# Kernel tuning notes

Measured on AMD Instinct MI355X. Metric: run time of the kernel, lower is better.

The kernel has to match this reference:

```python
import jax, jax.numpy as jnp
import numpy as np

N_NODES = 50000
N_EDGES = 600000
IN_C = 128
OUT_C = 128
N_REL = 8


def setup_inputs() -> dict:
    key = jax.random.key(0)
    k1, k2, k3, k4 = jax.random.split(key, 4)
    x = jax.random.normal(k1, (N_NODES, IN_C), dtype=jnp.float32)
    edge_index = jax.random.randint(k2, (2, N_EDGES), 0, N_NODES, dtype=jnp.int64)
    edge_type = jax.random.randint(k3, (N_EDGES,), 0, N_REL, dtype=jnp.int64)
    weight = jax.random.normal(k4, (N_REL, IN_C, OUT_C), dtype=jnp.float32)
    bias = jnp.zeros((OUT_C,), dtype=jnp.float32)
    return {"x": x, "edge_index": edge_index, "edge_type": edge_type,
            "weight": weight, "bias": bias}


def reference(x, edge_index, edge_type, weight, bias):
    # x: [N, in], edge_index: [2, E] (src, dst), edge_type: [E]
    # weight: [R, in, out], bias: [out]
    N = x.shape[0]
    src = edge_index[0]
    dst = edge_index[1]
    out = jnp.zeros((N, weight.shape[2]), dtype=x.dtype)
    for r in range(weight.shape[0]):
        rel_mask = (edge_type == r).astype(x.dtype)  # [E]
        transformed = x @ weight[r]                  # [N, out]
        msgs = transformed[src] * rel_mask[:, None]  # [E, out]
        sums = jax.ops.segment_sum(msgs, dst, num_segments=N)        # [N, out]
        counts = jax.ops.segment_sum(rel_mask, dst, num_segments=N)  # [N]
        mean = jnp.where(counts[:, None] > 0,
                         sums / jnp.maximum(counts, 1.0)[:, None],
                         0.0)
        out = out + mean
    return out + bias
```

## Files before the change

### kernel.cpp

```cpp
#include <hip/hip_runtime.h>
#include <hip/hip_bf16.h>


#define C128 128
#define BR 64

typedef __attribute__((ext_vector_type(8))) short short8;
typedef __attribute__((ext_vector_type(4))) float f32x4;

__device__ __forceinline__ void gload_lds16(void* lds, const void* gsrc) {
    __builtin_amdgcn_global_load_lds(
        (const __attribute__((address_space(1))) unsigned int*)gsrc,
        (__attribute__((address_space(3))) unsigned int*)lds, 16, 0, 0);
}

__device__ __forceinline__ float bf16u_f32(unsigned short u) {
    union { unsigned int i; float f; } c;
    c.i = ((unsigned int)u) << 16;
    return c.f;
}


__global__ __launch_bounds__(256) void pre_kernel(const int* __restrict__ ei,
                                                  const int* __restrict__ et,
                                                  unsigned* __restrict__ cursor,
                                                  const float* __restrict__ W,
                                                  __hip_bfloat16* __restrict__ WbT,
                                                  const float* __restrict__ x,
                                                  __hip_bfloat16* __restrict__ xb,
                                                  int n_edges, int n_nodes,
                                                  int hblk, int wblk, int wtot, int xt8) {
    int bid = blockIdx.x;
    if (bid < hblk) {
        int e = bid * 256 + threadIdx.x;
        if (e < n_edges)
            atomicAdd(&cursor[(size_t)et[e] * n_nodes + ei[n_edges + e]], 1u);
    } else if (bid < hblk + wblk) {
        int i = (bid - hblk) * 256 + threadIdx.x;
        if (i < wtot) {
            int r = i >> 14, k = (i >> 7) & 127, n = i & 127;
            WbT[(r << 14) + (n << 7) + ((((k >> 3) ^ (n & 7)) << 3) | (k & 7))] =
                __float2bfloat16(W[i]);
        }
    } else {
        int i = (bid - hblk - wblk) * 256 + threadIdx.x;
        if (i < xt8) {
            const float4* src = reinterpret_cast<const float4*>(x + (size_t)i * 8);
            float4 v0 = src[0], v1 = src[1];
            short8 o;
            o[0] = (short)__bfloat16_as_ushort(__float2bfloat16(v0.x));
            o[1] = (short)__bfloat16_as_ushort(__float2bfloat16(v0.y));
            o[2] = (short)__bfloat16_as_ushort(__float2bfloat16(v0.z));
            o[3] = (short)__bfloat16_as_ushort(__float2bfloat16(v0.w));
            o[4] = (short)__bfloat16_as_ushort(__float2bfloat16(v1.x));
            o[5] = (short)__bfloat16_as_ushort(__float2bfloat16(v1.y));
            o[6] = (short)__bfloat16_as_ushort(__float2bfloat16(v1.z));
            o[7] = (short)__bfloat16_as_ushort(__float2bfloat16(v1.w));
            *reinterpret_cast<short8*>(reinterpret_cast<unsigned short*>(xb) + (size_t)i * 8) = o;
        }
    }
}


__global__ __launch_bounds__(256) void scan1_kernel(const unsigned* __restrict__ cnt,
                                                    unsigned* __restrict__ part, int total) {
    __shared__ unsigned s[256];
    int t = threadIdx.x;
    int base = blockIdx.x * 1024 + t * 4;
    unsigned sum = 0;
#pragma unroll
    for (int i = 0; i < 4; ++i) {
        int idx = base + i;
        if (idx < total) sum += cnt[idx];
    }
    s[t] = sum;
    __syncthreads();
    for (int d = 128; d > 0; d >>= 1) {
        if (t < d) s[t] += s[t + d];
        __syncthreads();
    }
    if (t == 0) part[blockIdx.x] = s[0];
}

__global__ __launch_bounds__(512) void scan2_kernel(unsigned* __restrict__ part, int nblk) {
    __shared__ unsigned s[512];
    int t = threadIdx.x;
    unsigned run = 0;
    for (int base = 0; base < nblk; base += 512) {
        int i = base + t;
        unsigned v = (i < nblk) ? part[i] : 0u;
        s[t] = v;
        __syncthreads();
        for (int d = 1; d < 512; d <<= 1) {
            unsigned u = (t >= d) ? s[t - d] : 0u;
            __syncthreads();
            s[t] += u;
            __syncthreads();
        }
        unsigned incl = s[t];
        if (i < nblk) part[i] = run + incl - v;
        unsigned tot = s[511];
        __syncthreads();
        run += tot;
    }
}

__global__ __launch_bounds__(256) void scan3_kernel(unsigned* __restrict__ cursor,
                                                    unsigned* __restrict__ off,
                                                    const unsigned* __restrict__ part,
                                                    int total, int n_edges) {
    __shared__ unsigned s[256];
    int t = threadIdx.x;
    int base = blockIdx.x * 1024 + t * 4;
    unsigned v[4];
    unsigned tsum = 0;
#pragma unroll
    for (int i = 0; i < 4; ++i) {
        int idx = base + i;
        v[i] = (idx < total) ? cursor[idx] : 0u;
        tsum += v[i];
    }
    s[t] = tsum;
    __syncthreads();
    for (int d = 1; d < 256; d <<= 1) {
        unsigned u = (t >= d) ? s[t - d] : 0u;
        __syncthreads();
        s[t] += u;
        __syncthreads();
    }
    unsigned run = s[t] - tsum + part[blockIdx.x];
#pragma unroll
    for (int i = 0; i < 4; ++i) {
        int idx = base + i;
        if (idx < total) {
            off[idx] = run;
            cursor[idx] = run;
            run += v[i];
        }
    }
    if (blockIdx.x == 0 && t == 0) off[total] = (unsigned)n_edges;
}

__global__ __launch_bounds__(256) void place_kernel(const int* __restrict__ ei,
                                                    const int* __restrict__ et,
                                                    unsigned* __restrict__ cursor,
                                                    int* __restrict__ sorted_src,
                                                    int n_edges, int n_nodes) {
    int e = blockIdx.x * 256 + threadIdx.x;
    if (e < n_edges) {
        int src = ei[e];
        int dst = ei[n_edges + e];
        int key = et[e] * n_nodes + dst;
        unsigned pos = atomicAdd(&cursor[key], 1u);
        sorted_src[pos] = src;
    }
}


__global__ __launch_bounds__(256, 4) void fused_kernel(
    const __hip_bfloat16* __restrict__ xb, const int* __restrict__ ss,
    const unsigned* __restrict__ off, const __hip_bfloat16* __restrict__ WbT,
    const float* __restrict__ bias, float* __restrict__ out,
    int n_nodes, int n_rel) {
    __shared__ __align__(16) __hip_bfloat16 sW[C128 * C128];
    const int t = threadIdx.x, lane = t & 63, w = t >> 6;
    const int l16 = lane & 15, cg = lane >> 4;
    const int row0 = blockIdx.x * BR;
    const int rl = w * 16 + l16;
    const int node = row0 + rl;
    const unsigned short* xbu = reinterpret_cast<const unsigned short*>(xb);

    f32x4 acc[8];
#pragma unroll
    for (int i = 0; i < 8; ++i) acc[i] = (f32x4){0.f, 0.f, 0.f, 0.f};

    for (int p = 0; p < n_rel; ++p) {
        unsigned beg = 0, end = 0;
        if (node < n_nodes) {
            size_t key = (size_t)p * n_nodes + node;
            beg = off[key];
            end = off[key + 1];
        }
        const char* wp = (const char*)(WbT + ((size_t)p << 14));
#pragma unroll
        for (int i = 0; i < 8; ++i) {
            int seg = i * 4 + w;
            gload_lds16((char*)sW + seg * 1024 + lane * 16, wp + seg * 1024 + lane * 16);
        }
        float a[4][8];
#pragma unroll
        for (int kt = 0; kt < 4; ++kt)
#pragma unroll
            for (int j = 0; j < 8; ++j) a[kt][j] = 0.f;
        int n = (int)(end - beg);
        int e = (int)beg;
        int snx = (n > 0) ? ss[e] : 0;
        for (int i = 0; i < n; ++i) {
            int sv = snx;
            snx = (i + 1 < n) ? ss[e + i + 1] : 0;
            const unsigned short* rowp = xbu + ((size_t)sv << 7) + cg * 8;
            short8 v0 = *reinterpret_cast<const short8*>(rowp);
            short8 v1 = *reinterpret_cast<const short8*>(rowp + 32);
            short8 v2 = *reinterpret_cast<const short8*>(rowp + 64);
            short8 v3 = *reinterpret_cast<const short8*>(rowp + 96);
#pragma unroll
            for (int j = 0; j < 8; ++j) {
                a[0][j] += bf16u_f32((unsigned short)v0[j]);
                a[1][j] += bf16u_f32((unsigned short)v1[j]);
                a[2][j] += bf16u_f32((unsigned short)v2[j]);
                a[3][j] += bf16u_f32((unsigned short)v3[j]);
            }
        }
        float inv = (n > 0) ? 1.0f / (float)n : 0.0f;
        short8 af[4];
#pragma unroll
        for (int kt = 0; kt < 4; ++kt) {
            short8 o;
#pragma unroll
            for (int j = 0; j < 8; ++j)
                o[j] = (short)__bfloat16_as_ushort(__float2bfloat16(a[kt][j] * inv));
            af[kt] = o;
        }
        __syncthreads();

#pragma unroll
        for (int kt = 0; kt < 4; ++kt) {
            int chunk = kt * 4 + cg;
#pragma unroll
            for (int nt = 0; nt < 8; ++nt) {
                int wn = nt * 16 + l16;
                short8 bf = *reinterpret_cast<const short8*>(
                    &sW[(wn << 7) + ((chunk ^ (wn & 7)) << 3)]);
                acc[nt] = __builtin_amdgcn_mfma_f32_16x16x32_bf16(af[kt], bf, acc[nt], 0, 0, 0);
            }
        }
        __syncthreads();
    }

    const int rbase = row0 + w * 16 + (cg << 2);
#pragma unroll
    for (int nt = 0; nt < 8; ++nt) {
        int col = nt * 16 + l16;
        float b = bias[col];
#pragma unroll
        for (int i = 0; i < 4; ++i) {
            int r = rbase + i;
            if (r < n_nodes)
                out[(size_t)r * C128 + col] = acc[nt][i] + b;
        }
    }
}


static inline char* align16p(char* p) {
    return (char*)(((uintptr_t)p + 15) & ~(uintptr_t)15);
}

extern "C" void kernel_launch(void* const* d_in, const int* in_sizes, int n_in,
                              void* d_out, int out_size, void* d_ws, size_t ws_size,
                              hipStream_t stream) {
    const float* x    = (const float*)d_in[0];
    const int*   ei   = (const int*)d_in[1];
    const int*   et   = (const int*)d_in[2];
    const float* W    = (const float*)d_in[3];
    const float* bias = (const float*)d_in[4];
    float* out = (float*)d_out;

    const int n_nodes = in_sizes[0] / C128;
    const int n_edges = in_sizes[2];
    const int n_rel   = in_sizes[3] / (C128 * C128);
    const int RN = n_rel * n_nodes;

    char* p = (char*)d_ws;
    unsigned* off = (unsigned*)p;      p += (size_t)(RN + 1) * 4; p = align16p(p);
    unsigned* cursor = (unsigned*)p;   p += (size_t)RN * 4;       p = align16p(p);
    unsigned* part = (unsigned*)p;     p += 4096 * 4;
    int* sorted_src = (int*)p;         p += (size_t)n_edges * 4;  p = align16p(p);
    __hip_bfloat16* WbT = (__hip_bfloat16*)p; p += (size_t)n_rel * C128 * C128 * 2; p = align16p(p);
    __hip_bfloat16* xb = (__hip_bfloat16*)p;

    hipMemsetAsync(cursor, 0, (size_t)RN * 4, stream);

    int wtot = n_rel * C128 * C128;
    int xt8 = n_nodes * (C128 / 8);
    int hblk = (n_edges + 255) / 256;
    int wblk = (wtot + 255) / 256;
    int xblk = (xt8 + 255) / 256;
    pre_kernel<<<hblk + wblk + xblk, 256, 0, stream>>>(ei, et, cursor, W, WbT, x, xb,
                                                       n_edges, n_nodes, hblk, wblk, wtot, xt8);

    int nblk = (RN + 1023) / 1024;
    scan1_kernel<<<nblk, 256, 0, stream>>>(cursor, part, RN);
    scan2_kernel<<<1, 512, 0, stream>>>(part, nblk);
    scan3_kernel<<<nblk, 256, 0, stream>>>(cursor, off, part, RN, n_edges);
    place_kernel<<<(n_edges + 255) / 256, 256, 0, stream>>>(ei, et, cursor, sorted_src,
                                                            n_edges, n_nodes);

    int mblk = (n_nodes + BR - 1) / BR;
    fused_kernel<<<mblk, 256, 0, stream>>>(xb, sorted_src, off, WbT, bias, out,
                                           n_nodes, n_rel);
}
```

Before: 146.8 us.

## Merge scan kernels into cooperative launch and gather two relations concurrently

```diff
diff --git a/kernel.cpp b/kernel.cpp
--- a/kernel.cpp
+++ b/kernel.cpp
@@ -1,5 +1,8 @@
 #include <hip/hip_runtime.h>
 #include <hip/hip_bf16.h>
+#include <hip/hip_cooperative_groups.h>
+
+namespace cg = cooperative_groups;
 
 
 #define C128 128
@@ -62,83 +65,84 @@
 }
 
 
-__global__ __launch_bounds__(256) void scan1_kernel(const unsigned* __restrict__ cnt,
-                                                    unsigned* __restrict__ part, int total) {
+__global__ __launch_bounds__(256) void scan_kernel(unsigned* __restrict__ cursor,
+                                                   unsigned* __restrict__ off,
+                                                   unsigned* __restrict__ part,
+                                                   int total, int n_edges) {
+    cg::grid_group grid = cg::this_grid();
     __shared__ unsigned s[256];
-    int t = threadIdx.x;
-    int base = blockIdx.x * 1024 + t * 4;
-    unsigned sum = 0;
-#pragma unroll
-    for (int i = 0; i < 4; ++i) {
-        int idx = base + i;
-        if (idx < total) sum += cnt[idx];
-    }
-    s[t] = sum;
-    __syncthreads();
-    for (int d = 128; d > 0; d >>= 1) {
-        if (t < d) s[t] += s[t + d];
-        __syncthreads();
-    }
-    if (t == 0) part[blockIdx.x] = s[0];
-}
-
-__global__ __launch_bounds__(512) void scan2_kernel(unsigned* __restrict__ part, int nblk) {
-    __shared__ unsigned s[512];
-    int t = threadIdx.x;
-    unsigned run = 0;
-    for (int base = 0; base < nblk; base += 512) {
-        int i = base + t;
-        unsigned v = (i < nblk) ? part[i] : 0u;
-        s[t] = v;
-        __syncthreads();
-        for (int d = 1; d < 512; d <<= 1) {
+    const int t = threadIdx.x;
+    const int bid = blockIdx.x;
+    const int base = bid * 1024 + t * 4;
+
+    {
+        unsigned sum = 0;
+#pragma unroll
+        for (int i = 0; i < 4; ++i) {
+            int idx = base + i;
+            if (idx < total) sum += cursor[idx];
+        }
+        s[t] = sum;
+        __syncthreads();
+        for (int d = 128; d > 0; d >>= 1) {
+            if (t < d) s[t] += s[t + d];
+            __syncthreads();
+        }
+        if (t == 0) part[bid] = s[0];
+    }
+    grid.sync();
+
+    if (bid == 0) {
+        int nb = gridDim.x;
+        unsigned run = 0;
+        for (int b2 = 0; b2 < nb; b2 += 256) {
+            int i = b2 + t;
+            unsigned v = (i < nb) ? part[i] : 0u;
+            s[t] = v;
+            __syncthreads();
+            for (int d = 1; d < 256; d <<= 1) {
+                unsigned u = (t >= d) ? s[t - d] : 0u;
+                __syncthreads();
+                s[t] += u;
+                __syncthreads();
+            }
+            if (i < nb) part[i] = run + s[t] - v;
+            unsigned tot = s[255];
+            __syncthreads();
+            run += tot;
+        }
+    }
+    grid.sync();
+
+    {
+        unsigned v[4];
+        unsigned tsum = 0;
+#pragma unroll
+        for (int i = 0; i < 4; ++i) {
+            int idx = base + i;
+            v[i] = (idx < total) ? cursor[idx] : 0u;
+            tsum += v[i];
+        }
+        s[t] = tsum;
+        __syncthreads();
+        for (int d = 1; d < 256; d <<= 1) {
             unsigned u = (t >= d) ? s[t - d] : 0u;
             __syncthreads();
             s[t] += u;
             __syncthreads();
         }
-        unsigned incl = s[t];
-        if (i < nblk) part[i] = run + incl - v;
-        unsigned tot = s[511];
-        __syncthreads();
-        run += tot;
-    }
-}
-
-__global__ __launch_bounds__(256) void scan3_kernel(unsigned* __restrict__ cursor,
-                                                    unsigned* __restrict__ off,
-                                                    const unsigned* __restrict__ part,
-                                                    int total, int n_edges) {
-    __shared__ unsigned s[256];
-    int t = threadIdx.x;
-    int base = blockIdx.x * 1024 + t * 4;
-    unsigned v[4];
-    unsigned tsum = 0;
-#pragma unroll
-    for (int i = 0; i < 4; ++i) {
-        int idx = base + i;
-        v[i] = (idx < total) ? cursor[idx] : 0u;
-        tsum += v[i];
-    }
-    s[t] = tsum;
-    __syncthreads();
-    for (int d = 1; d < 256; d <<= 1) {
-        unsigned u = (t >= d) ? s[t - d] : 0u;
-        __syncthreads();
-        s[t] += u;
-        __syncthreads();
-    }
-    unsigned run = s[t] - tsum + part[blockIdx.x];
-#pragma unroll
-    for (int i = 0; i < 4; ++i) {
-        int idx = base + i;
-        if (idx < total) {
-            off[idx] = run;
-            cursor[idx] = run;
-            run += v[i];
-        }
-    }
-    if (blockIdx.x == 0 && t == 0) off[total] = (unsigned)n_edges;
+        unsigned run = s[t] - tsum + part[bid];
+#pragma unroll
+        for (int i = 0; i < 4; ++i) {
+            int idx = base + i;
+            if (idx < total) {
+                off[idx] = run;
+                cursor[idx] = run;
+                run += v[i];
+            }
+        }
+        if (bid == 0 && t == 0) off[total] = (unsigned)n_edges;
+    }
 }
 
 __global__ __launch_bounds__(256) void place_kernel(const int* __restrict__ ei,
@@ -157,7 +161,7 @@
 }
 
 
-__global__ __launch_bounds__(256, 4) void fused_kernel(
+__global__ __launch_bounds__(256, 3) void fused_kernel(
     const __hip_bfloat16* __restrict__ xb, const int* __restrict__ ss,
     const unsigned* __restrict__ off, const __hip_bfloat16* __restrict__ WbT,
     const float* __restrict__ bias, float* __restrict__ out,
@@ -168,72 +172,152 @@
     const int row0 = blockIdx.x * BR;
     const int rl = w * 16 + l16;
     const int node = row0 + rl;
+    const bool live = (node < n_nodes);
     const unsigned short* xbu = reinterpret_cast<const unsigned short*>(xb);
 
     f32x4 acc[8];
 #pragma unroll
     for (int i = 0; i < 8; ++i) acc[i] = (f32x4){0.f, 0.f, 0.f, 0.f};
 
-    for (int p = 0; p < n_rel; ++p) {
-        unsigned beg = 0, end = 0;
-        if (node < n_nodes) {
-            size_t key = (size_t)p * n_nodes + node;
-            beg = off[key];
-            end = off[key + 1];
-        }
-        const char* wp = (const char*)(WbT + ((size_t)p << 14));
-#pragma unroll
-        for (int i = 0; i < 8; ++i) {
-            int seg = i * 4 + w;
-            gload_lds16((char*)sW + seg * 1024 + lane * 16, wp + seg * 1024 + lane * 16);
-        }
-        float a[4][8];
+#define STAGE_W(P)                                                              \
+    {                                                                           \
+        const char* wp_ = (const char*)(WbT + ((size_t)(P) << 14));             \
+        _Pragma("unroll") for (int i_ = 0; i_ < 8; ++i_) {                      \
+            int seg_ = i_ * 4 + w;                                              \
+            gload_lds16((char*)sW + seg_ * 1024 + lane * 16,                    \
+                        wp_ + seg_ * 1024 + lane * 16);                         \
+        }                                                                       \
+    }
+
+#define MFMA_REL(AF)                                                            \
+    _Pragma("unroll") for (int kt_ = 0; kt_ < 4; ++kt_) {                       \
+        int chunk_ = kt_ * 4 + cg;                                              \
+        _Pragma("unroll") for (int nt_ = 0; nt_ < 8; ++nt_) {                   \
+            int wn_ = nt_ * 16 + l16;                                           \
+            short8 bf_ = *reinterpret_cast<const short8*>(                      \
+                &sW[(wn_ << 7) + ((chunk_ ^ (wn_ & 7)) << 3)]);                 \
+            acc[nt_] = __builtin_amdgcn_mfma_f32_16x16x32_bf16(AF[kt_], bf_,    \
+                                                               acc[nt_], 0, 0, 0); \
+        }                                                                       \
+    }
+
+    int p = 0;
+    for (; p + 1 < n_rel; p += 2) {
+        unsigned b0 = 0, e0 = 0, b1 = 0, e1 = 0;
+        if (live) {
+            size_t k0 = (size_t)p * n_nodes + node;
+            size_t k1 = k0 + (size_t)n_nodes;
+            b0 = off[k0]; e0 = off[k0 + 1];
+            b1 = off[k1]; e1 = off[k1 + 1];
+        }
+        STAGE_W(p);
+
+        int n0 = (int)(e0 - b0), n1 = (int)(e1 - b1);
+        int nm = n0 > n1 ? n0 : n1;
+        float a0[4][8], a1[4][8];
 #pragma unroll
         for (int kt = 0; kt < 4; ++kt)
 #pragma unroll
-            for (int j = 0; j < 8; ++j) a[kt][j] = 0.f;
-        int n = (int)(end - beg);
-        int e = (int)beg;
-        int snx = (n > 0) ? ss[e] : 0;
-        for (int i = 0; i < n; ++i) {
-            int sv = snx;
-            snx = (i + 1 < n) ? ss[e + i + 1] : 0;
-            const unsigned short* rowp = xbu + ((size_t)sv << 7) + cg * 8;
-            short8 v0 = *reinterpret_cast<const short8*>(rowp);
-            short8 v1 = *reinterpret_cast<const short8*>(rowp + 32);
-            short8 v2 = *reinterpret_cast<const short8*>(rowp + 64);
-            short8 v3 = *reinterpret_cast<const short8*>(rowp + 96);
+            for (int j = 0; j < 8; ++j) { a0[kt][j] = 0.f; a1[kt][j] = 0.f; }
+
+        int s0 = (n0 > 0) ? ss[b0] : 0;
+        int s1 = (n1 > 0) ? ss[b1] : 0;
+        for (int i = 0; i < nm; ++i) {
+            if (i < n0) {
+                const unsigned short* rp = xbu + ((size_t)s0 << 7) + cg * 8;
+                short8 v0 = *reinterpret_cast<const short8*>(rp);
+                short8 v1 = *reinterpret_cast<const short8*>(rp + 32);
+                short8 v2 = *reinterpret_cast<const short8*>(rp + 64);
+                short8 v3 = *reinterpret_cast<const short8*>(rp + 96);
+                s0 = (i + 1 < n0) ? ss[(int)b0 + i + 1] : 0;
+#pragma unroll
+                for (int j = 0; j < 8; ++j) {
+                    a0[0][j] += bf16u_f32((unsigned short)v0[j]);
+                    a0[1][j] += bf16u_f32((unsigned short)v1[j]);
+                    a0[2][j] += bf16u_f32((unsigned short)v2[j]);
+                    a0[3][j] += bf16u_f32((unsigned short)v3[j]);
+                }
+            }
+            if (i < n1) {
+                const unsigned short* rp = xbu + ((size_t)s1 << 7) + cg * 8;
+                short8 v0 = *reinterpret_cast<const short8*>(rp);
+                short8 v1 = *reinterpret_cast<const short8*>(rp + 32);
+                short8 v2 = *reinterpret_cast<const short8*>(rp + 64);
+                short8 v3 = *reinterpret_cast<const short8*>(rp + 96);
+                s1 = (i + 1 < n1) ? ss[(int)b1 + i + 1] : 0;
+#pragma unroll
+                for (int j = 0; j < 8; ++j) {
+                    a1[0][j] += bf16u_f32((unsigned short)v0[j]);
+                    a1[1][j] += bf16u_f32((unsigned short)v1[j]);
+                    a1[2][j] += bf16u_f32((unsigned short)v2[j]);
+                    a1[3][j] += bf16u_f32((unsigned short)v3[j]);
+                }
+            }
+        }
+        float i0 = (n0 > 0) ? 1.0f / (float)n0 : 0.0f;
+        float i1 = (n1 > 0) ? 1.0f / (float)n1 : 0.0f;
+        short8 af0[4], af1[4];
+#pragma unroll
+        for (int kt = 0; kt < 4; ++kt) {
+            short8 o0, o1;
 #pragma unroll
             for (int j = 0; j < 8; ++j) {
-                a[0][j] += bf16u_f32((unsigned short)v0[j]);
-                a[1][j] += bf16u_f32((unsigned short)v1[j]);
-                a[2][j] += bf16u_f32((unsigned short)v2[j]);
-                a[3][j] += bf16u_f32((unsigned short)v3[j]);
-            }
-        }
-        float inv = (n > 0) ? 1.0f / (float)n : 0.0f;
-        short8 af[4];
+                o0[j] = (short)__bfloat16_as_ushort(__float2bfloat16(a0[kt][j] * i0));
+                o1[j] = (short)__bfloat16_as_ushort(__float2bfloat16(a1[kt][j] * i1));
+            }
+            af0[kt] = o0;
+            af1[kt] = o1;
+        }
+
+        __syncthreads();
+        MFMA_REL(af0);
+        __syncthreads();
+        STAGE_W(p + 1);
+        __syncthreads();
+        MFMA_REL(af1);
+        __syncthreads();
+    }
+    if (p < n_rel) {
+        unsigned b0 = 0, e0 = 0;
+        if (live) {
+            size_t k0 = (size_t)p * n_nodes + node;
+            b0 = off[k0]; e0 = off[k0 + 1];
+        }
+        STAGE_W(p);
+        int n0 = (int)(e0 - b0);
+        float a0[4][8];
+#pragma unroll
+        for (int kt = 0; kt < 4; ++kt)
+#pragma unroll
+            for (int j = 0; j < 8; ++j) a0[kt][j] = 0.f;
+        int s0 = (n0 > 0) ? ss[b0] : 0;
+        for (int i = 0; i < n0; ++i) {
+            const unsigned short* rp = xbu + ((size_t)s0 << 7) + cg * 8;
+            short8 v0 = *reinterpret_cast<const short8*>(rp);
+            short8 v1 = *reinterpret_cast<const short8*>(rp + 32);
+            short8 v2 = *reinterpret_cast<const short8*>(rp + 64);
+            short8 v3 = *reinterpret_cast<const short8*>(rp + 96);
+            s0 = (i + 1 < n0) ? ss[(int)b0 + i + 1] : 0;
+#pragma unroll
+            for (int j = 0; j < 8; ++j) {
+                a0[0][j] += bf16u_f32((unsigned short)v0[j]);
+                a0[1][j] += bf16u_f32((unsigned short)v1[j]);
+                a0[2][j] += bf16u_f32((unsigned short)v2[j]);
+                a0[3][j] += bf16u_f32((unsigned short)v3[j]);
+            }
+        }
+        float i0 = (n0 > 0) ? 1.0f / (float)n0 : 0.0f;
+        short8 af0[4];
 #pragma unroll
         for (int kt = 0; kt < 4; ++kt) {
-            short8 o;
+            short8 o0;
 #pragma unroll
             for (int j = 0; j < 8; ++j)
-                o[j] = (short)__bfloat16_as_ushort(__float2bfloat16(a[kt][j] * inv));
-            af[kt] = o;
-        }
-        __syncthreads();
-
-#pragma unroll
-        for (int kt = 0; kt < 4; ++kt) {
-            int chunk = kt * 4 + cg;
-#pragma unroll
-            for (int nt = 0; nt < 8; ++nt) {
-                int wn = nt * 16 + l16;
-                short8 bf = *reinterpret_cast<const short8*>(
-                    &sW[(wn << 7) + ((chunk ^ (wn & 7)) << 3)]);
-                acc[nt] = __builtin_amdgcn_mfma_f32_16x16x32_bf16(af[kt], bf, acc[nt], 0, 0, 0);
-            }
-        }
+                o0[j] = (short)__bfloat16_as_ushort(__float2bfloat16(a0[kt][j] * i0));
+            af0[kt] = o0;
+        }
+        __syncthreads();
+        MFMA_REL(af0);
         __syncthreads();
     }
 
@@ -249,6 +333,8 @@
                 out[(size_t)r * C128 + col] = acc[nt][i] + b;
         }
     }
+#undef STAGE_W
+#undef MFMA_REL
 }
 
 
@@ -290,9 +376,16 @@
                                                        n_edges, n_nodes, hblk, wblk, wtot, xt8);
 
     int nblk = (RN + 1023) / 1024;
-    scan1_kernel<<<nblk, 256, 0, stream>>>(cursor, part, RN);
-    scan2_kernel<<<1, 512, 0, stream>>>(part, nblk);
-    scan3_kernel<<<nblk, 256, 0, stream>>>(cursor, off, part, RN, n_edges);
+    {
+        unsigned* cursor_a = cursor;
+        unsigned* off_a = off;
+        unsigned* part_a = part;
+        int RN_a = RN, ne_a = n_edges;
+        void* args[] = {(void*)&cursor_a, (void*)&off_a, (void*)&part_a,
+                        (void*)&RN_a, (void*)&ne_a};
+        hipLaunchCooperativeKernel((void*)scan_kernel, dim3(nblk), dim3(256), args, 0, stream);
+    }
+
     place_kernel<<<(n_edges + 255) / 256, 256, 0, stream>>>(ei, et, cursor, sorted_src,
                                                             n_edges, n_nodes);
 
```

Result: slower. 243.9 us (+66.2%).

## Drop LDS weight staging, use single-wave blocks, and fuse scan passes

Applied to the files above, without the earlier changes.

```diff
diff --git a/kernel.cpp b/kernel.cpp
--- a/kernel.cpp
+++ b/kernel.cpp
@@ -3,16 +3,10 @@
 
 
 #define C128 128
-#define BR 64
+#define BR 16
 
 typedef __attribute__((ext_vector_type(8))) short short8;
 typedef __attribute__((ext_vector_type(4))) float f32x4;
-
-__device__ __forceinline__ void gload_lds16(void* lds, const void* gsrc) {
-    __builtin_amdgcn_global_load_lds(
-        (const __attribute__((address_space(1))) unsigned int*)gsrc,
-        (__attribute__((address_space(3))) unsigned int*)lds, 16, 0, 0);
-}
 
 __device__ __forceinline__ float bf16u_f32(unsigned short u) {
     union { unsigned int i; float f; } c;
@@ -39,8 +33,10 @@
         int i = (bid - hblk) * 256 + threadIdx.x;
         if (i < wtot) {
             int r = i >> 14, k = (i >> 7) & 127, n = i & 127;
-            WbT[(r << 14) + (n << 7) + ((((k >> 3) ^ (n & 7)) << 3) | (k & 7))] =
-                __float2bfloat16(W[i]);
+            int kt = k >> 5, cg = (k >> 3) & 3, j = k & 7;
+            int nt = n >> 4, l16 = n & 15;
+            int pos = ((((r * 4 + kt) * 8 + nt) * 4 + cg) * 16 + l16) * 8 + j;
+            WbT[pos] = __float2bfloat16(W[i]);
         }
     } else {
         int i = (bid - hblk - wblk) * 256 + threadIdx.x;
@@ -82,36 +78,28 @@
     if (t == 0) part[blockIdx.x] = s[0];
 }
 
-__global__ __launch_bounds__(512) void scan2_kernel(unsigned* __restrict__ part, int nblk) {
-    __shared__ unsigned s[512];
-    int t = threadIdx.x;
-    unsigned run = 0;
-    for (int base = 0; base < nblk; base += 512) {
-        int i = base + t;
-        unsigned v = (i < nblk) ? part[i] : 0u;
-        s[t] = v;
-        __syncthreads();
-        for (int d = 1; d < 512; d <<= 1) {
-            unsigned u = (t >= d) ? s[t - d] : 0u;
+__global__ __launch_bounds__(256) void scan23_kernel(unsigned* __restrict__ cursor,
+                                                     unsigned* __restrict__ off,
+                                                     const unsigned* __restrict__ part,
+                                                     int total, int n_edges) {
+    __shared__ unsigned s[256];
+    const int t = threadIdx.x;
+    const int bid = blockIdx.x;
+
+    unsigned basesum = 0;
+    for (int i0 = 0; i0 < bid; i0 += 256) {
+        int i = i0 + t;
+        s[t] = (i < bid) ? part[i] : 0u;
+        __syncthreads();
+        for (int d = 128; d > 0; d >>= 1) {
+            if (t < d) s[t] += s[t + d];
             __syncthreads();
-            s[t] += u;
-            __syncthreads();
-        }
-        unsigned incl = s[t];
-        if (i < nblk) part[i] = run + incl - v;
-        unsigned tot = s[511];
-        __syncthreads();
-        run += tot;
-    }
-}
-
-__global__ __launch_bounds__(256) void scan3_kernel(unsigned* __restrict__ cursor,
-                                                    unsigned* __restrict__ off,
-                                                    const unsigned* __restrict__ part,
-                                                    int total, int n_edges) {
-    __shared__ unsigned s[256];
-    int t = threadIdx.x;
-    int base = blockIdx.x * 1024 + t * 4;
+        }
+        basesum += s[0];
+        __syncthreads();
+    }
+
+    int base = bid * 1024 + t * 4;
     unsigned v[4];
     unsigned tsum = 0;
 #pragma unroll
@@ -128,7 +116,7 @@
         s[t] += u;
         __syncthreads();
     }
-    unsigned run = s[t] - tsum + part[blockIdx.x];
+    unsigned run = s[t] - tsum + basesum;
 #pragma unroll
     for (int i = 0; i < 4; ++i) {
         int idx = base + i;
@@ -138,7 +126,7 @@
             run += v[i];
         }
     }
-    if (blockIdx.x == 0 && t == 0) off[total] = (unsigned)n_edges;
+    if (bid == 0 && t == 0) off[total] = (unsigned)n_edges;
 }
 
 __global__ __launch_bounds__(256) void place_kernel(const int* __restrict__ ei,
@@ -157,52 +145,51 @@
 }
 
 
-__global__ __launch_bounds__(256, 4) void fused_kernel(
+__global__ __launch_bounds__(64, 3) void fused_kernel(
     const __hip_bfloat16* __restrict__ xb, const int* __restrict__ ss,
     const unsigned* __restrict__ off, const __hip_bfloat16* __restrict__ WbT,
     const float* __restrict__ bias, float* __restrict__ out,
     int n_nodes, int n_rel) {
-    __shared__ __align__(16) __hip_bfloat16 sW[C128 * C128];
-    const int t = threadIdx.x, lane = t & 63, w = t >> 6;
+    const int lane = threadIdx.x & 63;
     const int l16 = lane & 15, cg = lane >> 4;
     const int row0 = blockIdx.x * BR;
-    const int rl = w * 16 + l16;
-    const int node = row0 + rl;
+    const int node = row0 + l16;
+    const bool live = (node < n_nodes);
     const unsigned short* xbu = reinterpret_cast<const unsigned short*>(xb);
+    const unsigned short* wpu = reinterpret_cast<const unsigned short*>(WbT);
 
     f32x4 acc[8];
 #pragma unroll
     for (int i = 0; i < 8; ++i) acc[i] = (f32x4){0.f, 0.f, 0.f, 0.f};
 
+    unsigned b = 0, e = 0;
+    if (live) { b = off[node]; e = off[node + 1]; }
+
     for (int p = 0; p < n_rel; ++p) {
-        unsigned beg = 0, end = 0;
-        if (node < n_nodes) {
-            size_t key = (size_t)p * n_nodes + node;
-            beg = off[key];
-            end = off[key + 1];
-        }
-        const char* wp = (const char*)(WbT + ((size_t)p << 14));
-#pragma unroll
-        for (int i = 0; i < 8; ++i) {
-            int seg = i * 4 + w;
-            gload_lds16((char*)sW + seg * 1024 + lane * 16, wp + seg * 1024 + lane * 16);
-        }
+        unsigned nb = 0, ne = 0;
+        if (p + 1 < n_rel && live) {
+            size_t k = (size_t)(p + 1) * n_nodes + node;
+            nb = off[k];
+            ne = off[k + 1];
+        }
+
         float a[4][8];
 #pragma unroll
         for (int kt = 0; kt < 4; ++kt)
 #pragma unroll
             for (int j = 0; j < 8; ++j) a[kt][j] = 0.f;
-        int n = (int)(end - beg);
-        int e = (int)beg;
-        int snx = (n > 0) ? ss[e] : 0;
-        for (int i = 0; i < n; ++i) {
-            int sv = snx;
-            snx = (i + 1 < n) ? ss[e + i + 1] : 0;
-            const unsigned short* rowp = xbu + ((size_t)sv << 7) + cg * 8;
-            short8 v0 = *reinterpret_cast<const short8*>(rowp);
-            short8 v1 = *reinterpret_cast<const short8*>(rowp + 32);
-            short8 v2 = *reinterpret_cast<const short8*>(rowp + 64);
-            short8 v3 = *reinterpret_cast<const short8*>(rowp + 96);
+
+        int n0 = (int)(e - b);
+        int eb = (int)b;
+        int s0 = (n0 > 0) ? ss[eb] : 0;
+        for (int i = 0; i < n0; ++i) {
+            int sv = s0;
+            s0 = (i + 1 < n0) ? ss[eb + i + 1] : 0;
+            const unsigned short* rp = xbu + ((size_t)sv << 7) + cg * 8;
+            short8 v0 = *reinterpret_cast<const short8*>(rp);
+            short8 v1 = *reinterpret_cast<const short8*>(rp + 32);
+            short8 v2 = *reinterpret_cast<const short8*>(rp + 64);
+            short8 v3 = *reinterpret_cast<const short8*>(rp + 96);
 #pragma unroll
             for (int j = 0; j < 8; ++j) {
                 a[0][j] += bf16u_f32((unsigned short)v0[j]);
@@ -211,7 +198,7 @@
                 a[3][j] += bf16u_f32((unsigned short)v3[j]);
             }
         }
-        float inv = (n > 0) ? 1.0f / (float)n : 0.0f;
+        float inv = (n0 > 0) ? 1.0f / (float)n0 : 0.0f;
         short8 af[4];
 #pragma unroll
         for (int kt = 0; kt < 4; ++kt) {
@@ -221,32 +208,34 @@
                 o[j] = (short)__bfloat16_as_ushort(__float2bfloat16(a[kt][j] * inv));
             af[kt] = o;
         }
-        __syncthreads();
 
 #pragma unroll
         for (int kt = 0; kt < 4; ++kt) {
-            int chunk = kt * 4 + cg;
-#pragma unroll
-            for (int nt = 0; nt < 8; ++nt) {
-                int wn = nt * 16 + l16;
-                short8 bf = *reinterpret_cast<const short8*>(
-                    &sW[(wn << 7) + ((chunk ^ (wn & 7)) << 3)]);
-                acc[nt] = __builtin_amdgcn_mfma_f32_16x16x32_bf16(af[kt], bf, acc[nt], 0, 0, 0);
-            }
-        }
-        __syncthreads();
-    }
-
-    const int rbase = row0 + w * 16 + (cg << 2);
+            short8 bf[8];
+#pragma unroll
+            for (int nt = 0; nt < 8; ++nt)
+                bf[nt] = *reinterpret_cast<const short8*>(
+                    wpu + ((size_t)(((p * 4 + kt) * 8 + nt) * 64 + lane)) * 8);
+#pragma unroll
+            for (int nt = 0; nt < 8; ++nt)
+                acc[nt] = __builtin_amdgcn_mfma_f32_16x16x32_bf16(af[kt], bf[nt],
+                                                                  acc[nt], 0, 0, 0);
+        }
+
+        b = nb;
+        e = ne;
+    }
+
+    const int rbase = row0 + (cg << 2);
 #pragma unroll
     for (int nt = 0; nt < 8; ++nt) {
         int col = nt * 16 + l16;
-        float b = bias[col];
+        float bv = bias[col];
 #pragma unroll
         for (int i = 0; i < 4; ++i) {
             int r = rbase + i;
             if (r < n_nodes)
-                out[(size_t)r * C128 + col] = acc[nt][i] + b;
+                out[(size_t)r * C128 + col] = acc[nt][i] + bv;
         }
     }
 }
@@ -291,12 +280,11 @@
 
     int nblk = (RN + 1023) / 1024;
     scan1_kernel<<<nblk, 256, 0, stream>>>(cursor, part, RN);
-    scan2_kernel<<<1, 512, 0, stream>>>(part, nblk);
-    scan3_kernel<<<nblk, 256, 0, stream>>>(cursor, off, part, RN, n_edges);
+    scan23_kernel<<<nblk, 256, 0, stream>>>(cursor, off, part, RN, n_edges);
     place_kernel<<<(n_edges + 255) / 256, 256, 0, stream>>>(ei, et, cursor, sorted_src,
                                                             n_edges, n_nodes);
 
     int mblk = (n_nodes + BR - 1) / BR;
-    fused_kernel<<<mblk, 256, 0, stream>>>(xb, sorted_src, off, WbT, bias, out,
-                                           n_nodes, n_rel);
-}
+    fused_kernel<<<mblk, 64, 0, stream>>>(xb, sorted_src, off, WbT, bias, out,
+                                          n_nodes, n_rel);
+}
```

After: 150.0 us. 2.2% more time.
